# Kernel optimization log

Measured on AMD Instinct MI355X. Metric: run time of the kernel, lower is better.

## Reference

```python
import jax, jax.numpy as jnp
import numpy as np

B, C, H, W = 8, 256, 64, 64
OUT, K = 256, 3
OG = 1
STRIDE, PAD, DIL = 1, 1, 1
K2 = K * K


def setup_inputs() -> dict:
    key = jax.random.key(0)
    ks = jax.random.split(key, 5)
    x = jax.random.normal(ks[0], (B, C, H, W), jnp.float32)
    # main deform-conv weight [out, in//groups, k, k]
    weight = jax.random.normal(ks[1], (OUT, C, K, K), jnp.float32) * (1.0 / np.sqrt(C * K2))
    bias = jax.random.normal(ks[2], (OUT,), jnp.float32) * 0.01
    # param_generator: 3x3 conv -> 3*OG*K*K channels (oh, ow, mask)
    pg_w = jax.random.normal(ks[3], (3 * OG * K2, C, 3, 3), jnp.float32) * 0.01
    pg_b = jax.random.normal(ks[4], (3 * OG * K2,), jnp.float32) * 0.01
    return {"x": x, "weight": weight, "bias": bias, "pg_w": pg_w, "pg_b": pg_b}


def _conv3x3(x, w, b):
    y = jax.lax.conv_general_dilated(
        x, w, (1, 1), [(1, 1), (1, 1)],
        dimension_numbers=("NCHW", "OIHW", "NCHW"))
    return y + b[None, :, None, None]


def _bilinear_gather(img, py, px):
    # img [B,C,H,W]; py,px [B,K2,Ho,Wo] -> [B,C,K2,Ho,Wo]
    # Zero padding outside the image (torchvision deform_conv2d semantics).
    Hh, Ww = img.shape[2], img.shape[3]
    y0 = jnp.floor(py)
    x0 = jnp.floor(px)
    dy = py - y0
    dx = px - x0
    imgf = img.reshape(img.shape[0], img.shape[1], Hh * Ww)
    out = jnp.zeros((img.shape[0], img.shape[1]) + py.shape[1:], img.dtype)
    corners = (
        (0, 0, (1 - dy) * (1 - dx)),
        (0, 1, (1 - dy) * dx),
        (1, 0, dy * (1 - dx)),
        (1, 1, dy * dx),
    )
    for oy, ox, wgt in corners:
        yy = y0 + oy
        xx = x0 + ox
        valid = (yy >= 0) & (yy < Hh) & (xx >= 0) & (xx < Ww)
        yi = jnp.clip(yy, 0, Hh - 1).astype(jnp.int32)
        xi = jnp.clip(xx, 0, Ww - 1).astype(jnp.int32)
        idx = yi * Ww + xi  # [B,K2,Ho,Wo]
        g = jax.vmap(lambda im, ix: jnp.take(im, ix.reshape(-1), axis=1))(imgf, idx)
        g = g.reshape(img.shape[0], img.shape[1], *idx.shape[1:])
        out = out + g * (wgt * valid)[:, None]
    return out


def _deform_conv2d(x, weight, bias, pg_w, pg_b):
    Bn = x.shape[0]
    Hi, Wi = x.shape[2], x.shape[3]
    Ho = (Hi + 2 * PAD - DIL * (K - 1) - 1) // STRIDE + 1
    Wo = (Wi + 2 * PAD - DIL * (K - 1) - 1) // STRIDE + 1
    params = _conv3x3(x, pg_w, pg_b)  # [B, 3*OG*K2, H, W]
    oh, ow, mask = jnp.split(params, 3, axis=1)
    offset = jnp.concatenate([oh, ow], axis=1)  # [B, 2*OG*K2, Ho, Wo]
    mask = jax.nn.sigmoid(mask)                  # [B, OG*K2, Ho, Wo]
    # torchvision layout: channel = ((og*K2 + k)*2 + {y,x})
    off = offset.reshape(Bn, OG, K2, 2, Ho, Wo)
    dy = off[:, :, :, 0].reshape(Bn, K2, Ho, Wo)  # OG == 1
    dx = off[:, :, :, 1].reshape(Bn, K2, Ho, Wo)
    hy = jnp.arange(Ho, dtype=x.dtype) * STRIDE - PAD
    wx = jnp.arange(Wo, dtype=x.dtype) * STRIDE - PAD
    ky, kx = jnp.meshgrid(jnp.arange(K), jnp.arange(K), indexing="ij")
    base_y = hy[None, :, None] + (ky.reshape(-1) * DIL).astype(x.dtype)[:, None, None]  # [K2,Ho,1]
    base_x = wx[None, None, :] + (kx.reshape(-1) * DIL).astype(x.dtype)[:, None, None]  # [K2,1,Wo]
    py = dy + base_y[None]  # [B,K2,Ho,Wo]
    px = dx + base_x[None]
    sampled = _bilinear_gather(x, py, px)          # [B,C,K2,Ho,Wo]
    sampled = sampled * mask[:, None]              # modulation (OG=1)
    out = jnp.einsum("bckhw,ock->bohw", sampled, weight.reshape(OUT, C, K2))
    return out + bias[None, :, None, None]


def reference(x, weight, bias, pg_w, pg_b):
    return _deform_conv2d(x, weight, bias, pg_w, pg_b)
```

## Files before the change

### kernel.cpp

```cpp
#include <hip/hip_runtime.h>
#include <math.h>

#define BQ   8
#define CIN  256
#define HH   64
#define WW   64
#define COUT 256
#define K2   9
#define PCH  27

#define PT     64
#define CCH    32
#define NCHUNK (CIN / CCH)
#define KSTEP  9
#define NSTEP  (NCHUNK * KSTEP)
#define SROW   328
#define PLANE  (HH * WW)

typedef __attribute__((ext_vector_type(8))) short short8;
typedef __attribute__((ext_vector_type(4))) float f32x4;
typedef __attribute__((ext_vector_type(2))) float f32x2;

static __device__ __forceinline__ unsigned short f2bf(float f) {
    unsigned u = __builtin_bit_cast(unsigned, f);
    u += 0x7fff + ((u >> 16) & 1);
    return (unsigned short)(u >> 16);
}
static __device__ __forceinline__ f32x2 up2(unsigned u) {
    f32x2 r;
    r[0] = __builtin_bit_cast(float, u << 16);
    r[1] = __builtin_bit_cast(float, u & 0xffff0000u);
    return r;
}
static __device__ __forceinline__ unsigned cvtpk(float lo, float hi) {
    unsigned r;
    asm("v_cvt_pk_bf16_f32 %0, %1, %2" : "=v"(r) : "v"(lo), "v"(hi));
    return r;
}

__global__ __launch_bounds__(256) void k_packw(const float* __restrict__ w,
                                               unsigned short* __restrict__ wp) {
    int t = blockIdx.x * 256 + threadIdx.x;
    if (t >= NSTEP * COUT * 4) return;
    int q = t & 3;
    int o = (t >> 2) & 255;
    int s = t >> 10;
    short8 sv;
#pragma unroll
    for (int j = 0; j < 8; ++j) {
        int pos   = s * 32 + q * 8 + j;
        int chunk = pos / (CCH * K2);
        int pl    = pos % (CCH * K2);
        int ktap  = pl >> 5;
        int c     = chunk * CCH + (pl & 31);
        sv[j] = (short)f2bf(w[(o * CIN + c) * K2 + ktap]);
    }
    *(short8*)(wp + (size_t)t * 8) = sv;
}

__global__ __launch_bounds__(256) void k_packpg(const float* __restrict__ pgw,
                                                unsigned short* __restrict__ wpg) {
    int t = blockIdx.x * 256 + threadIdx.x;
    if (t >= NSTEP * 32 * 4) return;
    int q = t & 3;
    int o = (t >> 2) & 31;
    int s = t >> 7;
    short8 sv;
#pragma unroll
    for (int j = 0; j < 8; ++j) {
        int pos   = s * 32 + q * 8 + j;
        int chunk = pos / (CCH * K2);
        int pl    = pos % (CCH * K2);
        int ktap  = pl >> 5;
        int c     = chunk * CCH + (pl & 31);
        sv[j] = (o < PCH) ? (short)f2bf(pgw[(size_t)(o * CIN + c) * K2 + ktap]) : (short)0;
    }
    *(short8*)(wpg + (size_t)t * 8) = sv;
}

__global__ __launch_bounds__(256) void k_xt(const float* __restrict__ x,
                                            unsigned short* __restrict__ xT) {
    __shared__ float tile[64][65];
    int blk = blockIdx.x;
    int cc  = blk & 3;
    int y   = (blk >> 2) & 63;
    int b   = blk >> 8;
    int t   = threadIdx.x;
    int c0  = cc * 64;

    const float* xp = x + ((size_t)(b * CIN + c0) * HH + y) * WW;
#pragma unroll
    for (int r = 0; r < 16; ++r) {
        int cl = r * 4 + (t >> 6);
        int xx = t & 63;
        tile[cl][xx] = xp[(size_t)cl * PLANE + xx];
    }
    __syncthreads();
    unsigned short* op = xT + ((size_t)b * PLANE + (size_t)y * WW) * CIN + c0;
#pragma unroll
    for (int r = 0; r < 16; ++r) {
        int xx = r * 4 + (t >> 6);
        int cl = t & 63;
        op[(size_t)xx * CIN + cl] = f2bf(tile[cl][xx]);
    }
}

__global__ __launch_bounds__(512, 4) void k_fused(const unsigned short* __restrict__ xT,
                                                  const unsigned short* __restrict__ wp,
                                                  const unsigned short* __restrict__ wpg,
                                                  const float* __restrict__ bias,
                                                  const float* __restrict__ pgb,
                                                  float* __restrict__ out) {
    __shared__ alignas(16) unsigned short s_samp[PT][SROW];
    __shared__ float4 s_wgt4[K2][PT];
    __shared__ int4   s_off4[K2][PT];
    __shared__ float  s_params[32][65];

    int blk = blockIdx.x;
    int b   = blk >> 6;
    int h   = blk & 63;
    int t   = threadIdx.x;

    int gp = t >> 3;
    int cg = t & 7;
    int wv = t >> 6;
    int lm = t & 15;
    int lq = (t >> 4) & 3;

    const char* xTb = (const char*)xT + (size_t)b * PLANE * CIN * 2;

    {
        int ipg = wv >> 2;
        int rpg = wv & 3;
        f32x4 accpg = (f32x4){0.f, 0.f, 0.f, 0.f};

        for (int ch = 0; ch < NCHUNK; ++ch) {
            int chof = ch * (CCH * 2) + cg * 8;
#pragma unroll
            for (int k = 0; k < K2; ++k) {
                int row = h + (k / 3) - 1;
                int col = gp + (k % 3) - 1;
                bool ok = ((unsigned)row < (unsigned)HH) & ((unsigned)col < (unsigned)WW);
                int pix = min(max(row, 0), HH - 1) * WW + min(max(col, 0), WW - 1);
                uint2 d = *(const uint2*)(xTb + ((size_t)pix * (CIN * 2) + chof));
                if (!ok) { d.x = 0; d.y = 0; }
                *(uint2*)&s_samp[gp][k * CCH + cg * 4] = d;
            }
            __syncthreads();
#pragma unroll
            for (int sl = 0; sl < KSTEP; ++sl) {
                const unsigned short* wrow = wpg + (size_t)(ch * KSTEP + sl) * 32 * 32;
                short8 a  = *(const short8*)(wrow + (ipg * 16 + lm) * 32 + lq * 8);
                short8 bf = *(const short8*)&s_samp[rpg * 16 + lm][sl * 32 + lq * 8];
                accpg = __builtin_amdgcn_mfma_f32_16x16x32_bf16(a, bf, accpg, 0, 0, 0);
            }
            __syncthreads();
        }
#pragma unroll
        for (int rg = 0; rg < 4; ++rg) {
            int oc = ipg * 16 + lq * 4 + rg;
            float bb = (oc < PCH) ? pgb[oc] : 0.f;
            s_params[oc][rpg * 16 + lm] = accpg[rg] + bb;
        }
    }
    __syncthreads();

    for (int e = t; e < K2 * PT; e += 512) {
        int k = e >> 6;
        int p = e & 63;
        float dy = s_params[2 * k][p];
        float dx = s_params[2 * k + 1][p];
        float mz = s_params[18 + k][p];
        float m  = 1.f / (1.f + expf(-mz));

        float py = dy + (float)(h - 1 + k / 3);
        float px = dx + (float)(p - 1 + k % 3);
        float y0f = floorf(py), x0f = floorf(px);
        float fy = py - y0f,    fx = px - x0f;
        int iy0 = (int)y0f, ix0 = (int)x0f;
        int iy1 = iy0 + 1,  ix1 = ix0 + 1;
        bool vy0 = (unsigned)iy0 < (unsigned)HH;
        bool vy1 = (unsigned)iy1 < (unsigned)HH;
        bool vx0 = (unsigned)ix0 < (unsigned)WW;
        bool vx1 = (unsigned)ix1 < (unsigned)WW;

        float w00 = (1.f - fy) * (1.f - fx) * m; if (!(vy0 && vx0)) w00 = 0.f;
        float w01 = (1.f - fy) * fx         * m; if (!(vy0 && vx1)) w01 = 0.f;
        float w10 = fy         * (1.f - fx) * m; if (!(vy1 && vx0)) w10 = 0.f;
        float w11 = fy         * fx         * m; if (!(vy1 && vx1)) w11 = 0.f;

        int cy0 = min(max(iy0, 0), HH - 1), cy1 = min(max(iy1, 0), HH - 1);
        int cx0 = min(max(ix0, 0), WW - 1), cx1 = min(max(ix1, 0), WW - 1);

        s_wgt4[k][p] = make_float4(w00, w01, w10, w11);
        s_off4[k][p] = make_int4((cy0 * WW + cx0) * 512, (cy0 * WW + cx1) * 512,
                                 (cy1 * WW + cx0) * 512, (cy1 * WW + cx1) * 512);
    }
    __syncthreads();

    int ow = wv * 32;
    f32x4 acc[2][4];
#pragma unroll
    for (int i = 0; i < 2; ++i)
#pragma unroll
        for (int j = 0; j < 4; ++j) acc[i][j] = (f32x4){0.f, 0.f, 0.f, 0.f};

    for (int ch = 0; ch < NCHUNK; ++ch) {
        int chof = ch * (CCH * 2) + cg * 8;
#pragma unroll
        for (int k = 0; k < K2; ++k) {
            int4   ob = s_off4[k][gp];
            float4 gw = s_wgt4[k][gp];
            uint2 d00 = *(const uint2*)(xTb + (ob.x + chof));
            uint2 d01 = *(const uint2*)(xTb + (ob.y + chof));
            uint2 d10 = *(const uint2*)(xTb + (ob.z + chof));
            uint2 d11 = *(const uint2*)(xTb + (ob.w + chof));
            f32x2 v01 = gw.x * up2(d00.x) + gw.y * up2(d01.x)
                      + gw.z * up2(d10.x) + gw.w * up2(d11.x);
            f32x2 v23 = gw.x * up2(d00.y) + gw.y * up2(d01.y)
                      + gw.z * up2(d10.y) + gw.w * up2(d11.y);
            uint2 pk;
            pk.x = cvtpk(v01[0], v01[1]);
            pk.y = cvtpk(v23[0], v23[1]);
            *(uint2*)&s_samp[gp][k * CCH + cg * 4] = pk;
        }
        __syncthreads();

#pragma unroll
        for (int sl = 0; sl < KSTEP; ++sl) {
            const unsigned short* wrow = wp + (size_t)(ch * KSTEP + sl) * COUT * 32;
            short8 a0 = *(const short8*)(wrow + (ow +  0 + lm) * 32 + lq * 8);
            short8 a1 = *(const short8*)(wrow + (ow + 16 + lm) * 32 + lq * 8);
            short8 b0 = *(const short8*)&s_samp[ 0 + lm][sl * 32 + lq * 8];
            short8 b1 = *(const short8*)&s_samp[16 + lm][sl * 32 + lq * 8];
            short8 b2 = *(const short8*)&s_samp[32 + lm][sl * 32 + lq * 8];
            short8 b3 = *(const short8*)&s_samp[48 + lm][sl * 32 + lq * 8];
            acc[0][0] = __builtin_amdgcn_mfma_f32_16x16x32_bf16(a0, b0, acc[0][0], 0, 0, 0);
            acc[0][1] = __builtin_amdgcn_mfma_f32_16x16x32_bf16(a0, b1, acc[0][1], 0, 0, 0);
            acc[0][2] = __builtin_amdgcn_mfma_f32_16x16x32_bf16(a0, b2, acc[0][2], 0, 0, 0);
            acc[0][3] = __builtin_amdgcn_mfma_f32_16x16x32_bf16(a0, b3, acc[0][3], 0, 0, 0);
            acc[1][0] = __builtin_amdgcn_mfma_f32_16x16x32_bf16(a1, b0, acc[1][0], 0, 0, 0);
            acc[1][1] = __builtin_amdgcn_mfma_f32_16x16x32_bf16(a1, b1, acc[1][1], 0, 0, 0);
            acc[1][2] = __builtin_amdgcn_mfma_f32_16x16x32_bf16(a1, b2, acc[1][2], 0, 0, 0);
            acc[1][3] = __builtin_amdgcn_mfma_f32_16x16x32_bf16(a1, b3, acc[1][3], 0, 0, 0);
        }
        __syncthreads();
    }

    float* ob = out + ((size_t)b * COUT) * PLANE + h * WW;
#pragma unroll
    for (int i = 0; i < 2; ++i) {
        int o0 = ow + i * 16 + lq * 4;
        f32x4 bv = *(const f32x4*)(bias + o0);
#pragma unroll
        for (int rg = 0; rg < 4; ++rg) {
#pragma unroll
            for (int j = 0; j < 4; ++j)
                ob[(size_t)(o0 + rg) * PLANE + j * 16 + lm] = acc[i][j][rg] + bv[rg];
        }
    }
}

extern "C" void kernel_launch(void* const* d_in, const int* in_sizes, int n_in,
                              void* d_out, int out_size, void* d_ws, size_t ws_size,
                              hipStream_t stream) {
    const float* x    = (const float*)d_in[0];
    const float* wgt  = (const float*)d_in[1];
    const float* bias = (const float*)d_in[2];
    const float* pgw  = (const float*)d_in[3];
    const float* pgb  = (const float*)d_in[4];
    float* out = (float*)d_out;

    const size_t WPK_B = (size_t)NSTEP * COUT * 32 * 2;
    const size_t WPG_B = (size_t)NSTEP * 32 * 32 * 2;
    unsigned short* wpk = (unsigned short*)d_ws;
    unsigned short* wpg = (unsigned short*)((char*)d_ws + WPK_B);
    unsigned short* xT  = (unsigned short*)((char*)d_ws + WPK_B + WPG_B);

    k_packw <<<(NSTEP * COUT * 4 + 255) / 256, 256, 0, stream>>>(wgt, wpk);
    k_packpg<<<(NSTEP * 32 * 4 + 255) / 256,   256, 0, stream>>>(pgw, wpg);
    k_xt    <<<BQ * HH * 4, 256, 0, stream>>>(x, xT);
    k_fused <<<BQ * HH, 512, 0, stream>>>(xT, wpk, wpg, bias, pgb, out);
}
```

Before: 122.9 us.

## Software-pipeline gather and MFMA with double-buffered LDS and register prefetch

Both the param-generator conv loop and the main deform-conv loop now use a double-buffered shared sample tile. Global gathers for chunk ch+2 are held in registers while chunk ch+1 is written to the spare buffer, interleaved with the MFMAs on chunk ch. Weight fragments are prefetched one slice ahead, and s_setprio raises priority around the MFMA groups. This cuts one barrier per chunk and hides gather latency, at the cost of doubling LDS, adding many registers (launch bounds drop from 4 to 2 blocks per CU), and lowering occupancy.

```diff
diff --git a/kernel.cpp b/kernel.cpp
--- a/kernel.cpp
+++ b/kernel.cpp
@@ -105,13 +105,13 @@
     }
 }
 
-__global__ __launch_bounds__(512, 4) void k_fused(const unsigned short* __restrict__ xT,
+__global__ __launch_bounds__(512, 2) void k_fused(const unsigned short* __restrict__ xT,
                                                   const unsigned short* __restrict__ wp,
                                                   const unsigned short* __restrict__ wpg,
                                                   const float* __restrict__ bias,
                                                   const float* __restrict__ pgb,
                                                   float* __restrict__ out) {
-    __shared__ alignas(16) unsigned short s_samp[PT][SROW];
+    __shared__ alignas(16) unsigned short s_samp[2][PT][SROW];
     __shared__ float4 s_wgt4[K2][PT];
     __shared__ int4   s_off4[K2][PT];
     __shared__ float  s_params[32][65];
@@ -132,30 +132,67 @@
     {
         int ipg = wv >> 2;
         int rpg = wv & 3;
-        f32x4 accpg = (f32x4){0.f, 0.f, 0.f, 0.f};
+        f32x4 accA = (f32x4){0.f, 0.f, 0.f, 0.f};
+        f32x4 accB = (f32x4){0.f, 0.f, 0.f, 0.f};
+
+        int  pixo[K2];
+        bool okk[K2];
+#pragma unroll
+        for (int k = 0; k < K2; ++k) {
+            int row = h + (k / 3) - 1;
+            int col = gp + (k % 3) - 1;
+            okk[k]  = ((unsigned)row < (unsigned)HH) & ((unsigned)col < (unsigned)WW);
+            int pix = min(max(row, 0), HH - 1) * WW + min(max(col, 0), WW - 1);
+            pixo[k] = pix * (CIN * 2) + cg * 8;
+        }
+
+        uint2 Ga[K2];
+#pragma unroll
+        for (int k = 0; k < K2; ++k)
+            Ga[k] = *(const uint2*)(xTb + pixo[k]);
+#pragma unroll
+        for (int k = 0; k < K2; ++k) {
+            uint2 d = Ga[k];
+            if (!okk[k]) { d.x = 0; d.y = 0; }
+            *(uint2*)&s_samp[0][gp][k * CCH + cg * 4] = d;
+        }
+#pragma unroll
+        for (int k = 0; k < K2; ++k)
+            Ga[k] = *(const uint2*)(xTb + pixo[k] + (CCH * 2));
+        asm volatile("s_waitcnt lgkmcnt(0)" ::: "memory");
+        __builtin_amdgcn_s_barrier();
 
         for (int ch = 0; ch < NCHUNK; ++ch) {
-            int chof = ch * (CCH * 2) + cg * 8;
-#pragma unroll
-            for (int k = 0; k < K2; ++k) {
-                int row = h + (k / 3) - 1;
-                int col = gp + (k % 3) - 1;
-                bool ok = ((unsigned)row < (unsigned)HH) & ((unsigned)col < (unsigned)WW);
-                int pix = min(max(row, 0), HH - 1) * WW + min(max(col, 0), WW - 1);
-                uint2 d = *(const uint2*)(xTb + ((size_t)pix * (CIN * 2) + chof));
-                if (!ok) { d.x = 0; d.y = 0; }
-                *(uint2*)&s_samp[gp][k * CCH + cg * 4] = d;
+            bool doC = (ch + 1 < NCHUNK);
+            bool doL = (ch + 2 < NCHUNK);
+            unsigned short (*__restrict__ bc)[SROW] = s_samp[ch & 1];
+            unsigned short (*__restrict__ bn)[SROW] = s_samp[(ch + 1) & 1];
+            const unsigned short* wb = wpg + (size_t)(ch * KSTEP) * 32 * 32;
+            short8 ac = *(const short8*)(wb + (ipg * 16 + lm) * 32 + lq * 8);
+#pragma unroll
+            for (int sl = 0; sl < KSTEP; ++sl) {
+                short8 bf = *(const short8*)&bc[rpg * 16 + lm][sl * 32 + lq * 8];
+                short8 an = ac;
+                if (sl + 1 < KSTEP)
+                    an = *(const short8*)(wb + (size_t)(sl + 1) * 32 * 32
+                                          + (ipg * 16 + lm) * 32 + lq * 8);
+                if (doC) {
+                    uint2 d = Ga[sl];
+                    if (!okk[sl]) { d.x = 0; d.y = 0; }
+                    *(uint2*)&bn[gp][sl * CCH + cg * 4] = d;
+                }
+                if (doL)
+                    Ga[sl] = *(const uint2*)(xTb + pixo[sl] + (ch + 2) * (CCH * 2));
+                if (sl & 1)
+                    accB = __builtin_amdgcn_mfma_f32_16x16x32_bf16(ac, bf, accB, 0, 0, 0);
+                else
+                    accA = __builtin_amdgcn_mfma_f32_16x16x32_bf16(ac, bf, accA, 0, 0, 0);
+                ac = an;
             }
-            __syncthreads();
-#pragma unroll
-            for (int sl = 0; sl < KSTEP; ++sl) {
-                const unsigned short* wrow = wpg + (size_t)(ch * KSTEP + sl) * 32 * 32;
-                short8 a  = *(const short8*)(wrow + (ipg * 16 + lm) * 32 + lq * 8);
-                short8 bf = *(const short8*)&s_samp[rpg * 16 + lm][sl * 32 + lq * 8];
-                accpg = __builtin_amdgcn_mfma_f32_16x16x32_bf16(a, bf, accpg, 0, 0, 0);
-            }
-            __syncthreads();
-        }
+            asm volatile("s_waitcnt lgkmcnt(0)" ::: "memory");
+            __builtin_amdgcn_s_barrier();
+        }
+        f32x4 accpg = accA + accB;
 #pragma unroll
         for (int rg = 0; rg < 4; ++rg) {
             int oc = ipg * 16 + lq * 4 + rg;
@@ -205,46 +242,95 @@
 #pragma unroll
         for (int j = 0; j < 4; ++j) acc[i][j] = (f32x4){0.f, 0.f, 0.f, 0.f};
 
-    for (int ch = 0; ch < NCHUNK; ++ch) {
-        int chof = ch * (CCH * 2) + cg * 8;
-#pragma unroll
-        for (int k = 0; k < K2; ++k) {
-            int4   ob = s_off4[k][gp];
+    uint2 G[K2][4];
+    {
+        const int c0 = cg * 8;
+#pragma unroll
+        for (int k = 0; k < K2; ++k) {
+            int4 ob = s_off4[k][gp];
+            G[k][0] = *(const uint2*)(xTb + ob.x + c0);
+            G[k][1] = *(const uint2*)(xTb + ob.y + c0);
+            G[k][2] = *(const uint2*)(xTb + ob.z + c0);
+            G[k][3] = *(const uint2*)(xTb + ob.w + c0);
+        }
+#pragma unroll
+        for (int k = 0; k < K2; ++k) {
             float4 gw = s_wgt4[k][gp];
-            uint2 d00 = *(const uint2*)(xTb + (ob.x + chof));
-            uint2 d01 = *(const uint2*)(xTb + (ob.y + chof));
-            uint2 d10 = *(const uint2*)(xTb + (ob.z + chof));
-            uint2 d11 = *(const uint2*)(xTb + (ob.w + chof));
-            f32x2 v01 = gw.x * up2(d00.x) + gw.y * up2(d01.x)
-                      + gw.z * up2(d10.x) + gw.w * up2(d11.x);
-            f32x2 v23 = gw.x * up2(d00.y) + gw.y * up2(d01.y)
-                      + gw.z * up2(d10.y) + gw.w * up2(d11.y);
+            f32x2 v01 = gw.x * up2(G[k][0].x) + gw.y * up2(G[k][1].x)
+                      + gw.z * up2(G[k][2].x) + gw.w * up2(G[k][3].x);
+            f32x2 v23 = gw.x * up2(G[k][0].y) + gw.y * up2(G[k][1].y)
+                      + gw.z * up2(G[k][2].y) + gw.w * up2(G[k][3].y);
             uint2 pk;
             pk.x = cvtpk(v01[0], v01[1]);
             pk.y = cvtpk(v23[0], v23[1]);
-            *(uint2*)&s_samp[gp][k * CCH + cg * 4] = pk;
-        }
-        __syncthreads();
-
+            *(uint2*)&s_samp[0][gp][k * CCH + cg * 4] = pk;
+        }
+        const int c1 = (CCH * 2) + cg * 8;
+#pragma unroll
+        for (int k = 0; k < K2; ++k) {
+            int4 ob = s_off4[k][gp];
+            G[k][0] = *(const uint2*)(xTb + ob.x + c1);
+            G[k][1] = *(const uint2*)(xTb + ob.y + c1);
+            G[k][2] = *(const uint2*)(xTb + ob.z + c1);
+            G[k][3] = *(const uint2*)(xTb + ob.w + c1);
+        }
+        asm volatile("s_waitcnt lgkmcnt(0)" ::: "memory");
+        __builtin_amdgcn_s_barrier();
+    }
+
+    for (int ch = 0; ch < NCHUNK; ++ch) {
+        bool doC = (ch + 1 < NCHUNK);
+        bool doL = (ch + 2 < NCHUNK);
+        const int cofl = (ch + 2) * (CCH * 2) + cg * 8;
+        unsigned short (*__restrict__ bc)[SROW] = s_samp[ch & 1];
+        unsigned short (*__restrict__ bn)[SROW] = s_samp[(ch + 1) & 1];
+        const unsigned short* wb = wp + (size_t)(ch * KSTEP) * COUT * 32;
+        short8 a0c = *(const short8*)(wb + (ow +  0 + lm) * 32 + lq * 8);
+        short8 a1c = *(const short8*)(wb + (ow + 16 + lm) * 32 + lq * 8);
 #pragma unroll
         for (int sl = 0; sl < KSTEP; ++sl) {
-            const unsigned short* wrow = wp + (size_t)(ch * KSTEP + sl) * COUT * 32;
-            short8 a0 = *(const short8*)(wrow + (ow +  0 + lm) * 32 + lq * 8);
-            short8 a1 = *(const short8*)(wrow + (ow + 16 + lm) * 32 + lq * 8);
-            short8 b0 = *(const short8*)&s_samp[ 0 + lm][sl * 32 + lq * 8];
-            short8 b1 = *(const short8*)&s_samp[16 + lm][sl * 32 + lq * 8];
-            short8 b2 = *(const short8*)&s_samp[32 + lm][sl * 32 + lq * 8];
-            short8 b3 = *(const short8*)&s_samp[48 + lm][sl * 32 + lq * 8];
-            acc[0][0] = __builtin_amdgcn_mfma_f32_16x16x32_bf16(a0, b0, acc[0][0], 0, 0, 0);
-            acc[0][1] = __builtin_amdgcn_mfma_f32_16x16x32_bf16(a0, b1, acc[0][1], 0, 0, 0);
-            acc[0][2] = __builtin_amdgcn_mfma_f32_16x16x32_bf16(a0, b2, acc[0][2], 0, 0, 0);
-            acc[0][3] = __builtin_amdgcn_mfma_f32_16x16x32_bf16(a0, b3, acc[0][3], 0, 0, 0);
-            acc[1][0] = __builtin_amdgcn_mfma_f32_16x16x32_bf16(a1, b0, acc[1][0], 0, 0, 0);
-            acc[1][1] = __builtin_amdgcn_mfma_f32_16x16x32_bf16(a1, b1, acc[1][1], 0, 0, 0);
-            acc[1][2] = __builtin_amdgcn_mfma_f32_16x16x32_bf16(a1, b2, acc[1][2], 0, 0, 0);
-            acc[1][3] = __builtin_amdgcn_mfma_f32_16x16x32_bf16(a1, b3, acc[1][3], 0, 0, 0);
-        }
-        __syncthreads();
+            short8 b0 = *(const short8*)&bc[ 0 + lm][sl * 32 + lq * 8];
+            short8 b1 = *(const short8*)&bc[16 + lm][sl * 32 + lq * 8];
+            short8 b2 = *(const short8*)&bc[32 + lm][sl * 32 + lq * 8];
+            short8 b3 = *(const short8*)&bc[48 + lm][sl * 32 + lq * 8];
+            short8 a0n = a0c, a1n = a1c;
+            if (sl + 1 < KSTEP) {
+                const unsigned short* wrn = wb + (size_t)(sl + 1) * COUT * 32;
+                a0n = *(const short8*)(wrn + (ow +  0 + lm) * 32 + lq * 8);
+                a1n = *(const short8*)(wrn + (ow + 16 + lm) * 32 + lq * 8);
+            }
+            if (doC) {
+                float4 gw = s_wgt4[sl][gp];
+                f32x2 v01 = gw.x * up2(G[sl][0].x) + gw.y * up2(G[sl][1].x)
+                          + gw.z * up2(G[sl][2].x) + gw.w * up2(G[sl][3].x);
+                f32x2 v23 = gw.x * up2(G[sl][0].y) + gw.y * up2(G[sl][1].y)
+                          + gw.z * up2(G[sl][2].y) + gw.w * up2(G[sl][3].y);
+                uint2 pk;
+                pk.x = cvtpk(v01[0], v01[1]);
+                pk.y = cvtpk(v23[0], v23[1]);
+                *(uint2*)&bn[gp][sl * CCH + cg * 4] = pk;
+            }
+            if (doL) {
+                int4 ob = s_off4[sl][gp];
+                G[sl][0] = *(const uint2*)(xTb + ob.x + cofl);
+                G[sl][1] = *(const uint2*)(xTb + ob.y + cofl);
+                G[sl][2] = *(const uint2*)(xTb + ob.z + cofl);
+                G[sl][3] = *(const uint2*)(xTb + ob.w + cofl);
+            }
+            __builtin_amdgcn_s_setprio(1);
+            acc[0][0] = __builtin_amdgcn_mfma_f32_16x16x32_bf16(a0c, b0, acc[0][0], 0, 0, 0);
+            acc[0][1] = __builtin_amdgcn_mfma_f32_16x16x32_bf16(a0c, b1, acc[0][1], 0, 0, 0);
+            acc[0][2] = __builtin_amdgcn_mfma_f32_16x16x32_bf16(a0c, b2, acc[0][2], 0, 0, 0);
+            acc[0][3] = __builtin_amdgcn_mfma_f32_16x16x32_bf16(a0c, b3, acc[0][3], 0, 0, 0);
+            acc[1][0] = __builtin_amdgcn_mfma_f32_16x16x32_bf16(a1c, b0, acc[1][0], 0, 0, 0);
+            acc[1][1] = __builtin_amdgcn_mfma_f32_16x16x32_bf16(a1c, b1, acc[1][1], 0, 0, 0);
+            acc[1][2] = __builtin_amdgcn_mfma_f32_16x16x32_bf16(a1c, b2, acc[1][2], 0, 0, 0);
+            acc[1][3] = __builtin_amdgcn_mfma_f32_16x16x32_bf16(a1c, b3, acc[1][3], 0, 0, 0);
+            __builtin_amdgcn_s_setprio(0);
+            a0c = a0n; a1c = a1n;
+        }
+        asm volatile("s_waitcnt lgkmcnt(0)" ::: "memory");
+        __builtin_amdgcn_s_barrier();
     }
 
     float* ob = out + ((size_t)b * COUT) * PLANE + h * WW;
```

Result: slower. 125.9 us (+2.5%).
